# Kernel optimization log

Measured on AMD Instinct MI355X. Metric: run time of the kernel, lower is better.

Reference implementation:

```python
import jax, jax.numpy as jnp
import numpy as np

D_MODEL = 1024
N_HEADS = 16
D_HEAD = D_MODEL // N_HEADS
WINDOW = 256
DILATION = 1
GLOBAL_IDX = (0,)
NEG_INF = float('-inf')


def longformer_mask(seq_len):
    # Vectorized version of the original O(S^2) Python-loop mask builder.
    i = jnp.arange(seq_len)[:, None]
    j = jnp.arange(seq_len)[None, :]
    d = jnp.abs(i - j)
    window_ok = (d <= WINDOW) & (d % DILATION == 0)  # includes diagonal (d==0)
    is_global = jnp.zeros((seq_len,), dtype=bool).at[jnp.array(GLOBAL_IDX)].set(True)
    global_ok = is_global[:, None] | is_global[None, :]
    return jnp.where(window_ok | global_ok, 0.0, NEG_INF).astype(jnp.float32)


def setup_inputs() -> dict:
    key = jax.random.key(0)
    ks = jax.random.split(key, 9)
    s = 1.0 / np.sqrt(D_MODEL)
    inp = {'x': jax.random.normal(ks[0], (2, 2048, D_MODEL), dtype=jnp.float32)}
    for n, kw, kb in (('q', ks[1], ks[2]), ('k', ks[3], ks[4]), ('v', ks[5], ks[6]), ('o', ks[7], ks[8])):
        inp['W' + n] = jax.random.uniform(kw, (D_MODEL, D_MODEL), jnp.float32, -s, s)
        inp['b' + n] = jax.random.uniform(kb, (D_MODEL,), jnp.float32, -s, s)
    return inp


def reference(x, Wq, bq, Wk, bk, Wv, bv, Wo, bo):
    B, S, _ = x.shape
    scale = D_HEAD ** -0.5

    def split_heads(t):  # [B,S,D] -> [B,H,S,d]
        return t.reshape(B, S, N_HEADS, D_HEAD).transpose(0, 2, 1, 3)

    Q = split_heads(x @ Wq + bq)
    K = split_heads(x @ Wk + bk)
    V = split_heads(x @ Wv + bv)

    scores = jnp.einsum('bhqd,bhkd->bhqk', Q, K) * scale
    scores = scores + longformer_mask(S)[None, None]
    attn = jax.nn.softmax(scores, axis=-1)  # dropout is identity in eval
    out = jnp.einsum('bhqk,bhkd->bhqd', attn, V)
    out = out.transpose(0, 2, 1, 3).reshape(B, S, D_MODEL)
    return out @ Wo + bo
```

## Files before the change

kernel.cpp:

```cpp
#include <hip/hip_runtime.h>
#include <hip/hip_bf16.h>

typedef __attribute__((ext_vector_type(8))) short short8;
typedef __attribute__((ext_vector_type(4))) float floatx4;
typedef __attribute__((ext_vector_type(8))) _Float16 half8;
typedef __attribute__((ext_vector_type(4))) _Float16 half4;

using bf16 = __hip_bfloat16;
using fp16 = _Float16;

#define S_LEN 2048
#define DM 1024
#define NH 16
#define DH 64
#define WIN 256

__device__ __forceinline__ unsigned short f2b(float f) {
  __hip_bfloat16 h = __float2bfloat16(f);
  return *reinterpret_cast<unsigned short*>(&h);
}
__device__ __forceinline__ unsigned short f2h(float f) {
  fp16 h = (fp16)f;
  return *reinterpret_cast<unsigned short*>(&h);
}
__device__ __forceinline__ void lds_load16(void* lds, const void* gptr) {
  __builtin_amdgcn_global_load_lds(
      (const __attribute__((address_space(1))) unsigned int*)gptr,
      (__attribute__((address_space(3))) unsigned int*)lds, 16, 0, 0);
}

__global__ __launch_bounds__(256) void k_prep(const float* __restrict__ x,
                                              const float* __restrict__ W0,
                                              const float* __restrict__ W1,
                                              const float* __restrict__ W2,
                                              const float* __restrict__ W3,
                                              bf16* __restrict__ wT,
                                              ushort4* __restrict__ xb) {
  const int tx = threadIdx.x, ty = threadIdx.y;
  if (blockIdx.z == 4) {
    const int tid = ty * 32 + tx;
    const int blk = blockIdx.y * 32 + blockIdx.x;
    const float4* in4 = (const float4*)x;
    #pragma unroll
    for (int k = 0; k < 4; ++k) {
      int i = k * 262144 + blk * 256 + tid;
      float4 v = in4[i];
      ushort4 o;
      o.x = f2b(v.x); o.y = f2b(v.y); o.z = f2b(v.z); o.w = f2b(v.w);
      xb[i] = o;
    }
    return;
  }
  __shared__ float t[32][33];
  const float* W = (blockIdx.z == 0) ? W0 : (blockIdx.z == 1) ? W1 : (blockIdx.z == 2) ? W2 : W3;
  bf16* O = wT + (size_t)blockIdx.z * 1024 * 1024;
  int x0 = blockIdx.x * 32, y0 = blockIdx.y * 32;
  #pragma unroll
  for (int i = 0; i < 32; i += 8) t[ty + i][tx] = W[(size_t)(y0 + ty + i) * 1024 + x0 + tx];
  __syncthreads();
  #pragma unroll
  for (int i = 0; i < 32; i += 8)
    O[(size_t)(x0 + ty + i) * 1024 + y0 + tx] = __float2bfloat16(t[tx][ty + i]);
}

__global__ __launch_bounds__(512) void k_qkv(const bf16* __restrict__ A,
                                             const bf16* __restrict__ Bt,
                                             const float* __restrict__ bias_q,
                                             const float* __restrict__ bias_k,
                                             const float* __restrict__ bias_v,
                                             fp16* __restrict__ Qh, fp16* __restrict__ Kh,
                                             fp16* __restrict__ Vt) {
  __shared__ __align__(16) char lds[131072];
  const int tid = threadIdx.x;
  const int wave = tid >> 6, lane = tid & 63;
  const int ln = lane & 15, quad = lane >> 4;
  const int wr = wave >> 2, wc = wave & 3;

  const int gi = blockIdx.x;
  const int wg = (gi & 7) * 24 + (gi >> 3);
  const int mt = wg / 12, nt = wg % 12;

  auto mkF = [](int p) {
    int q = p ^ (((p >> 9) & 1) << 5);
    int sub = q >> 10;
    int w = q & 1023;
    return (((sub >> 1) << 4) + (w >> 6)) * 2048 + (sub & 1) * 64 + (w & 63);
  };
  const int F0 = mkF(tid * 16);
  const int F1 = mkF(8192 + tid * 16);
  const char* Ab = (const char*)A + (size_t)mt * 524288;
  const char* Bb = (const char*)Bt + (size_t)nt * 524288;

  auto stg = [&](int region, const char* g) {
    lds_load16(lds + region + wave * 1024, g + F0);
    lds_load16(lds + region + 8192 + wave * 1024, g + F1);
  };

  stg(0, Ab);
  stg(16384, Ab + 262144);
  stg(32768, Bb);
  stg(49152, Bb + 262144);
  stg(65536, Ab + 128);
  stg(65536 + 16384, Ab + 262144 + 128);
  stg(65536 + 32768, Bb + 128);
  stg(65536 + 49152, Bb + 262144 + 128);

  floatx4 acc[8][4];
  #pragma unroll
  for (int i = 0; i < 8; ++i)
    #pragma unroll
    for (int j = 0; j < 4; ++j) acc[i][j] = (floatx4){0.f, 0.f, 0.f, 0.f};

  const int lnq = ln * 64 + ((quad * 16) ^ ((ln & 8) << 2));
  const int aoff = wr * 16384 + lnq;
  const int boff = 32768 + (wc >> 1) * 16384 + (wc & 1) * 8192 + lnq;

  asm volatile("s_waitcnt vmcnt(8)" ::: "memory");
  __builtin_amdgcn_s_barrier();

  for (int t = 0; t < 16; ++t) {
    const char* bb = lds + ((t & 1) << 16);
    const int sreg = (t & 1) << 16;
    const char* gA = Ab + (t + 2) * 128;
    const char* gB = Bb + (t + 2) * 128;
    const bool pf = (t + 2 < 16);

    short8 a0[4][2], b0[4][2];
    #pragma unroll
    for (int m2 = 0; m2 < 4; ++m2)
      #pragma unroll
      for (int kk = 0; kk < 2; ++kk)
        a0[m2][kk] = *(const short8*)(bb + aoff + m2 * 2048 + kk * 1024);
    #pragma unroll
    for (int n2 = 0; n2 < 2; ++n2)
      #pragma unroll
      for (int kk = 0; kk < 2; ++kk)
        b0[n2][kk] = *(const short8*)(bb + boff + n2 * 2048 + kk * 1024);
    __builtin_amdgcn_s_barrier();
    __builtin_amdgcn_s_setprio(1);
    #pragma unroll
    for (int m2 = 0; m2 < 4; ++m2)
      #pragma unroll
      for (int n2 = 0; n2 < 2; ++n2) {
        acc[m2][n2] = __builtin_amdgcn_mfma_f32_16x16x32_bf16(a0[m2][0], b0[n2][0], acc[m2][n2], 0, 0, 0);
        acc[m2][n2] = __builtin_amdgcn_mfma_f32_16x16x32_bf16(a0[m2][1], b0[n2][1], acc[m2][n2], 0, 0, 0);
      }
    __builtin_amdgcn_s_setprio(0);
    __builtin_amdgcn_s_barrier();

    #pragma unroll
    for (int n2 = 2; n2 < 4; ++n2)
      #pragma unroll
      for (int kk = 0; kk < 2; ++kk)
        b0[n2][kk] = *(const short8*)(bb + boff + n2 * 2048 + kk * 1024);
    __builtin_amdgcn_s_barrier();
    __builtin_amdgcn_s_setprio(1);
    #pragma unroll
    for (int m2 = 0; m2 < 4; ++m2)
      #pragma unroll
      for (int n2 = 2; n2 < 4; ++n2) {
        acc[m2][n2] = __builtin_amdgcn_mfma_f32_16x16x32_bf16(a0[m2][0], b0[n2][0], acc[m2][n2], 0, 0, 0);
        acc[m2][n2] = __builtin_amdgcn_mfma_f32_16x16x32_bf16(a0[m2][1], b0[n2][1], acc[m2][n2], 0, 0, 0);
      }
    __builtin_amdgcn_s_setprio(0);
    __builtin_amdgcn_s_barrier();

    short8 a1[4][2];
    #pragma unroll
    for (int m2 = 0; m2 < 4; ++m2)
      #pragma unroll
      for (int kk = 0; kk < 2; ++kk)
        a1[m2][kk] = *(const short8*)(bb + aoff + (4 + m2) * 2048 + kk * 1024);
    if (pf) {
      stg(sreg + 32768, gB);
      stg(sreg + 49152, gB + 262144);
    }
    __builtin_amdgcn_s_barrier();
    __builtin_amdgcn_s_setprio(1);
    #pragma unroll
    for (int m2 = 0; m2 < 4; ++m2)
      #pragma unroll
      for (int n2 = 0; n2 < 2; ++n2) {
        acc[4 + m2][n2] = __builtin_amdgcn_mfma_f32_16x16x32_bf16(a1[m2][0], b0[n2][0], acc[4 + m2][n2], 0, 0, 0);
        acc[4 + m2][n2] = __builtin_amdgcn_mfma_f32_16x16x32_bf16(a1[m2][1], b0[n2][1], acc[4 + m2][n2], 0, 0, 0);
      }
    __builtin_amdgcn_s_setprio(0);
    __builtin_amdgcn_s_barrier();

    if (pf) {
      stg(sreg, gA);
      stg(sreg + 16384, gA + 262144);
      asm volatile("s_waitcnt vmcnt(8)" ::: "memory");
    } else {
      asm volatile("s_waitcnt vmcnt(0)" ::: "memory");
    }
    __builtin_amdgcn_s_barrier();
    __builtin_amdgcn_s_setprio(1);
    #pragma unroll
    for (int m2 = 0; m2 < 4; ++m2)
      #pragma unroll
      for (int n2 = 2; n2 < 4; ++n2) {
        acc[4 + m2][n2] = __builtin_amdgcn_mfma_f32_16x16x32_bf16(a1[m2][0], b0[n2][0], acc[4 + m2][n2], 0, 0, 0);
        acc[4 + m2][n2] = __builtin_amdgcn_mfma_f32_16x16x32_bf16(a1[m2][1], b0[n2][1], acc[4 + m2][n2], 0, 0, 0);
      }
    __builtin_amdgcn_s_setprio(0);
    __builtin_amdgcn_s_barrier();
  }

  const int g = nt >> 2;
  if (g == 2) {
    #pragma unroll
    for (int ni = 0; ni < 4; ++ni) {
      int nn = (nt & 3) * 256 + wc * 64 + ni * 16 + ln;
      int h = nn >> 6, dd = nn & 63;
      float bias = bias_v[nn];
      #pragma unroll
      for (int mi = 0; mi < 8; ++mi) {
        int m = mt * 256 + wr * 128 + mi * 16 + quad * 4;
        int b = m >> 11, s = m & 2047;
        ushort4 pk;
        pk.x = f2h(acc[mi][ni][0] + bias);
        pk.y = f2h(acc[mi][ni][1] + bias);
        pk.z = f2h(acc[mi][ni][2] + bias);
        pk.w = f2h(acc[mi][ni][3] + bias);
        *(ushort4*)&Vt[((size_t)((b * NH + h) * DH + dd)) * S_LEN + s] = pk;
      }
    }
  } else {
    const float* bp = (g == 0) ? bias_q : bias_k;
    fp16* og = (g == 0) ? Qh : Kh;
    #pragma unroll
    for (int ni = 0; ni < 4; ++ni) {
      int nn = (nt & 3) * 256 + wc * 64 + ni * 16 + ln;
      int h = nn >> 6, dd = nn & 63;
      float bias = bp[nn];
      #pragma unroll
      for (int mi = 0; mi < 8; ++mi) {
        #pragma unroll
        for (int r = 0; r < 4; ++r) {
          int m = mt * 256 + wr * 128 + mi * 16 + quad * 4 + r;
          int b = m >> 11, s = m & 2047;
          og[(size_t)((b * NH + h) * S_LEN + s) * DH + dd] = (fp16)(acc[mi][ni][r] + bias);
        }
      }
    }
  }
}

template <int MODE>
__global__ __launch_bounds__(256) void k_gemm(const bf16* __restrict__ A,
                                              const bf16* __restrict__ Bt,
                                              const float* __restrict__ bias_q,
                                              const float* __restrict__ bias_k,
                                              const float* __restrict__ bias_v,
                                              fp16* __restrict__ Qh, fp16* __restrict__ Kh,
                                              fp16* __restrict__ Vt, float* __restrict__ outF) {
  __shared__ __align__(16) bf16 As[2][128 * 32];
  __shared__ __align__(16) bf16 Bs[2][128 * 32];
  const int tid = threadIdx.x;
  const int wave = tid >> 6, lane = tid & 63;
  const int gi = blockIdx.x;
  const int xcd = gi & 7, grr = gi >> 3;
  const int m0 = (xcd * 4 + (grr & 3)) * 128;
  const int n0 = (grr >> 2) * 128;
  const int r0 = tid >> 2;
  const int cb = (tid & 3) * 16;
  const char* Ag = (const char*)A + (size_t)(m0 + r0) * 2048 + cb;
  const char* Bg = (const char*)Bt + (size_t)(n0 + r0) * 2048 + cb;
  char* As0W = (char*)&As[0][0] + wave * 1024;
  char* As1W = (char*)&As[1][0] + wave * 1024;
  char* Bs0W = (char*)&Bs[0][0] + wave * 1024;
  char* Bs1W = (char*)&Bs[1][0] + wave * 1024;
  const int wm = (wave & 1) * 64, wn = (wave >> 1) * 64;
  const int ln = lane & 15, quad = lane >> 4;

  floatx4 acc[4][4];
  #pragma unroll
  for (int i = 0; i < 4; i++)
    #pragma unroll
    for (int j = 0; j < 4; j++) acc[i][j] = (floatx4){0.f, 0.f, 0.f, 0.f};

  for (int k0 = 0; k0 < 1024; k0 += 64) {
    __syncthreads();
    lds_load16(As0W,        Ag + k0 * 2);
    lds_load16(As0W + 4096, Ag + 64 * 2048 + k0 * 2);
    lds_load16(As1W,        Ag + k0 * 2 + 64);
    lds_load16(As1W + 4096, Ag + 64 * 2048 + k0 * 2 + 64);
    lds_load16(Bs0W,        Bg + k0 * 2);
    lds_load16(Bs0W + 4096, Bg + 64 * 2048 + k0 * 2);
    lds_load16(Bs1W,        Bg + k0 * 2 + 64);
    lds_load16(Bs1W + 4096, Bg + 64 * 2048 + k0 * 2 + 64);
    __syncthreads();
    short8 af0[4], af1[4], bf0[4], bf1[4];
    #pragma unroll
    for (int mi = 0; mi < 4; mi++) {
      af0[mi] = *(const short8*)&As[0][(wm + mi * 16 + ln) * 32 + quad * 8];
      af1[mi] = *(const short8*)&As[1][(wm + mi * 16 + ln) * 32 + quad * 8];
    }
    #pragma unroll
    for (int ni = 0; ni < 4; ni++) {
      bf0[ni] = *(const short8*)&Bs[0][(wn + ni * 16 + ln) * 32 + quad * 8];
      bf1[ni] = *(const short8*)&Bs[1][(wn + ni * 16 + ln) * 32 + quad * 8];
    }
    #pragma unroll
    for (int mi = 0; mi < 4; mi++)
      #pragma unroll
      for (int ni = 0; ni < 4; ni++) {
        acc[mi][ni] = __builtin_amdgcn_mfma_f32_16x16x32_bf16(af0[mi], bf0[ni], acc[mi][ni], 0, 0, 0);
        acc[mi][ni] = __builtin_amdgcn_mfma_f32_16x16x32_bf16(af1[mi], bf1[ni], acc[mi][ni], 0, 0, 0);
      }
  }

  if constexpr (MODE == 0) {
    #pragma unroll
    for (int ni = 0; ni < 4; ni++) {
      int n = n0 + wn + ni * 16 + ln;
      int g = n >> 10, nn = n & 1023;
      int h = nn >> 6, dd = nn & 63;
      if (g == 2) {
        float bias = bias_v[nn];
        #pragma unroll
        for (int mi = 0; mi < 4; mi++) {
          int m = m0 + wm + mi * 16 + quad * 4;
          int b = m >> 11, s = m & 2047;
          ushort4 pk;
          pk.x = f2h(acc[mi][ni][0] + bias);
          pk.y = f2h(acc[mi][ni][1] + bias);
          pk.z = f2h(acc[mi][ni][2] + bias);
          pk.w = f2h(acc[mi][ni][3] + bias);
          *(ushort4*)&Vt[((size_t)(b * NH + h) * DH + dd) * S_LEN + s] = pk;
        }
      } else {
        const float* bp = (g == 0) ? bias_q : bias_k;
        fp16* og = (g == 0) ? Qh : Kh;
        float bias = bp[nn];
        #pragma unroll
        for (int mi = 0; mi < 4; mi++) {
          #pragma unroll
          for (int r = 0; r < 4; r++) {
            int m = m0 + wm + mi * 16 + quad * 4 + r;
            int b = m >> 11, s = m & 2047;
            og[(size_t)((b * NH + h) * S_LEN + s) * DH + dd] = (fp16)(acc[mi][ni][r] + bias);
          }
        }
      }
    }
  } else {
    #pragma unroll
    for (int ni = 0; ni < 4; ni++) {
      int n = n0 + wn + ni * 16 + ln;
      float bias = bias_q[n];
      #pragma unroll
      for (int mi = 0; mi < 4; mi++)
        #pragma unroll
        for (int r = 0; r < 4; r++) {
          int m = m0 + wm + mi * 16 + quad * 4 + r;
          outF[(size_t)m * 1024 + n] = acc[mi][ni][r] + bias;
        }
    }
  }
}

__global__ __launch_bounds__(256, 4) void k_attn(const fp16* __restrict__ Qh,
                                                 const fp16* __restrict__ Kh,
                                                 const fp16* __restrict__ Vt,
                                                 bf16* __restrict__ aout) {
  __shared__ __align__(16) fp16 KsL[2][64 * 72];
  __shared__ __align__(16) fp16 VsL[2][64 * 72];

  const int i = blockIdx.x;
  const int xcd = i & 7, rr = i >> 3;
  const int bh = xcd * 4 + (rr & 3);
  const int tile = rr >> 2;
  const int b = bh >> 4, h = bh & 15;
  const size_t base = (size_t)bh * S_LEN * DH;
  const fp16* Qp = Qh + base;
  const fp16* Kp = Kh + base;
  const fp16* Vp = Vt + base;
  const float SC2 = 0.18033688011112042f;
  const int tid = threadIdx.x;

  if (tile == 32) {
    float* sP = (float*)&KsL[0][0];
    float* oR = (float*)&VsL[0][0];
    float* red = (float*)&VsL[1][0];
    const int wv = tid >> 6, lane = tid & 63;
    const int g = lane >> 3, e8 = lane & 7;
    const half8 q0t = *(const half8*)(Qp + e8 * 8);
    float lsum = 0.f;
    for (int it = 0; it < 64; ++it) {
      int grp = wv * 64 + it;
      const half8 kv = *(const half8*)(Kp + (size_t)(grp * 8 + g) * DH + e8 * 8);
      float p = 0.f;
      #pragma unroll
      for (int e = 0; e < 8; ++e) p += (float)q0t[e] * (float)kv[e];
      p += __shfl_xor(p, 1, 64);
      p += __shfl_xor(p, 2, 64);
      p += __shfl_xor(p, 4, 64);
      p = exp2f(fmaf(p, SC2, -8.f));
      if (e8 == 0) sP[grp * 8 + g] = p;
      lsum += p;
    }
    #pragma unroll
    for (int off = 1; off < 64; off <<= 1) lsum += __shfl_xor(lsum, off, 64);
    if (lane == 0) red[wv] = lsum;
    __syncthreads();
    const float ltot = (red[0] + red[1] + red[2] + red[3]) * 0.125f;
    const int d = tid & 63, qu = tid >> 6;
    float o = 0.f;
    for (int j0 = qu * 512; j0 < qu * 512 + 512; j0 += 8) {
      half8 vv = *(const half8*)(Vp + (size_t)d * S_LEN + j0);
      #pragma unroll
      for (int e = 0; e < 8; ++e) o += sP[j0 + e] * (float)vv[e];
    }
    oR[tid] = o;
    __syncthreads();
    if (tid < 64) {
      float oo = oR[tid] + oR[tid + 64] + oR[tid + 128] + oR[tid + 192];
      aout[(size_t)(b * S_LEN) * DM + h * DH + tid] = __float2bfloat16(oo / ltot);
    }
    return;
  }

  const int w = tid >> 6, lane = tid & 63;
  const int ln = lane & 15, quad = lane >> 4;
  const int qb = tile * 64;
  const int qw = qb + w * 16;

  const half8 bq0 = *(const half8*)(Qp + (size_t)(qw + ln) * DH + quad * 8);
  const half8 bq1 = *(const half8*)(Qp + (size_t)(qw + ln) * DH + 32 + quad * 8);

  floatx4 acc[4];
  float l_i;

  {
    const half8 k0a = *(const half8*)(Kp + quad * 8);
    const half8 k0b = *(const half8*)(Kp + 32 + quad * 8);
    float s0 = 0.f;
    #pragma unroll
    for (int e = 0; e < 8; ++e)
      s0 += (float)bq0[e] * (float)k0a[e] + (float)bq1[e] * (float)k0b[e];
    s0 += __shfl_xor(s0, 16, 64);
    s0 += __shfl_xor(s0, 32, 64);
    float p0 = exp2f(fmaf(s0, SC2, -8.f));
    l_i = (quad == 0) ? p0 : 0.f;
    #pragma unroll
    for (int dt = 0; dt < 4; ++dt)
      #pragma unroll
      for (int r = 0; r < 4; ++r)
        acc[dt][r] = p0 * (float)Vp[(size_t)(dt * 16 + quad * 4 + r) * S_LEN];
  }

  int cs = qb - WIN; if (cs < 0) cs = 0;
  int ce = qb + 64 + WIN; if (ce > S_LEN) ce = S_LEN;

  const int f0 = tid, f1 = tid + 256;
  const int r0s = f0 >> 3, c0s = (f0 & 7) * 8;
  const int r1s = f1 >> 3, c1s = (f1 & 7) * 8;

  uint4 kreg0, kreg1, vreg0, vreg1;
  auto stage_load = [&](int c) {
    kreg0 = *(const uint4*)(Kp + (size_t)(c + r0s) * DH + c0s);
    kreg1 = *(const uint4*)(Kp + (size_t)(c + r1s) * DH + c1s);
    vreg0 = *(const uint4*)(Vp + (size_t)r0s * S_LEN + c + c0s);
    vreg1 = *(const uint4*)(Vp + (size_t)r1s * S_LEN + c + c1s);
  };
  auto stage_write = [&](int buf) {
    *(uint4*)&KsL[buf][r0s * 72 + c0s] = kreg0;
    *(uint4*)&KsL[buf][r1s * 72 + c1s] = kreg1;
    *(uint4*)&VsL[buf][r0s * 72 + c0s] = vreg0;
    *(uint4*)&VsL[buf][r1s * 72 + c1s] = vreg1;
  };

  auto compute = [&](int c, int buf) {
    floatx4 s[4];
    #pragma unroll
    for (int jt = 0; jt < 4; ++jt) {
      half8 k0 = *(const half8*)&KsL[buf][(jt * 16 + ln) * 72 + quad * 8];
      half8 k1 = *(const half8*)&KsL[buf][(jt * 16 + ln) * 72 + 32 + quad * 8];
      floatx4 z = (floatx4){0.f, 0.f, 0.f, 0.f};
      z = __builtin_amdgcn_mfma_f32_16x16x32_f16(k0, bq0, z, 0, 0, 0);
      s[jt] = __builtin_amdgcn_mfma_f32_16x16x32_f16(k1, bq1, z, 0, 0, 0);
    }
    half4 v01[8];
    #pragma unroll
    for (int dt = 0; dt < 2; ++dt)
      #pragma unroll
      for (int jt = 0; jt < 4; ++jt)
        v01[dt * 4 + jt] =
            *(const half4*)&VsL[buf][(dt * 16 + ln) * 72 + jt * 16 + quad * 4];
    const bool full_in = (c != 0) && (c >= qw - 241) && (c <= qw + 193);
    half4 Pt[4];
    if (full_in) {
      #pragma unroll
      for (int jt = 0; jt < 4; ++jt)
        #pragma unroll
        for (int r = 0; r < 4; ++r) {
          float pe = exp2f(fmaf(s[jt][r], SC2, -8.f));
          Pt[jt][r] = (fp16)pe;
          l_i += pe;
        }
    } else {
      const int q = qw + ln;
      #pragma unroll
      for (int jt = 0; jt < 4; ++jt) {
        #pragma unroll
        for (int r = 0; r < 4; ++r) {
          int j = c + jt * 16 + quad * 4 + r;
          int dq = q - j;
          bool ok = (dq <= WIN && dq >= -WIN) && (j != 0);
          float pe = ok ? exp2f(fmaf(s[jt][r], SC2, -8.f)) : 0.f;
          Pt[jt][r] = (fp16)pe;
          l_i += pe;
        }
      }
    }
    half4 v23[8];
    #pragma unroll
    for (int dt = 0; dt < 2; ++dt)
      #pragma unroll
      for (int jt = 0; jt < 4; ++jt)
        v23[dt * 4 + jt] =
            *(const half4*)&VsL[buf][((dt + 2) * 16 + ln) * 72 + jt * 16 + quad * 4];
    #pragma unroll
    for (int jt = 0; jt < 4; ++jt) {
      acc[0] = __builtin_amdgcn_mfma_f32_16x16x16f16(v01[jt], Pt[jt], acc[0], 0, 0, 0);
      acc[1] = __builtin_amdgcn_mfma_f32_16x16x16f16(v01[4 + jt], Pt[jt], acc[1], 0, 0, 0);
    }
    #pragma unroll
    for (int jt = 0; jt < 4; ++jt) {
      acc[2] = __builtin_amdgcn_mfma_f32_16x16x16f16(v23[jt], Pt[jt], acc[2], 0, 0, 0);
      acc[3] = __builtin_amdgcn_mfma_f32_16x16x16f16(v23[4 + jt], Pt[jt], acc[3], 0, 0, 0);
    }
  };

  stage_load(cs);
  stage_write(0);
  __syncthreads();
  int buf = 0;
  for (int c = cs; c < ce; c += 64) {
    const bool hasnext = (c + 64 < ce);
    if (hasnext) stage_load(c + 64);
    compute(c, buf);
    if (hasnext) stage_write(buf ^ 1);
    __syncthreads();
    buf ^= 1;
  }

  float lt = l_i;
  lt += __shfl_xor(lt, 16, 64);
  lt += __shfl_xor(lt, 32, 64);
  const float inv = 1.0f / lt;
  const int q = qw + ln;
  if (q != 0) {
    #pragma unroll
    for (int dt = 0; dt < 4; ++dt) {
      ushort4 pk;
      pk.x = f2b(acc[dt][0] * inv);
      pk.y = f2b(acc[dt][1] * inv);
      pk.z = f2b(acc[dt][2] * inv);
      pk.w = f2b(acc[dt][3] * inv);
      *(ushort4*)&aout[(size_t)(b * S_LEN + q) * DM + h * DH + dt * 16 + quad * 4] = pk;
    }
  }
}

extern "C" void kernel_launch(void* const* d_in, const int* in_sizes, int n_in,
                              void* d_out, int out_size, void* d_ws, size_t ws_size,
                              hipStream_t stream) {
  const float* x  = (const float*)d_in[0];
  const float* Wq = (const float*)d_in[1];
  const float* bq = (const float*)d_in[2];
  const float* Wk = (const float*)d_in[3];
  const float* bk = (const float*)d_in[4];
  const float* Wv = (const float*)d_in[5];
  const float* bv = (const float*)d_in[6];
  const float* Wo = (const float*)d_in[7];
  const float* bo = (const float*)d_in[8];
  float* out = (float*)d_out;

  const size_t SEG = (size_t)4096 * 1024;
  bf16* xb = (bf16*)d_ws;
  bf16* wT = xb + SEG;
  fp16* Qh = (fp16*)(wT + SEG);
  fp16* Kh = Qh + SEG;
  fp16* Vt = Kh + SEG;
  bf16* ao = (bf16*)(Vt + SEG);

  k_prep<<<dim3(32, 32, 5), dim3(32, 8), 0, stream>>>(x, Wq, Wk, Wv, Wo, wT, (ushort4*)xb);
  k_qkv<<<dim3(192), dim3(512), 0, stream>>>(xb, wT, bq, bk, bv, Qh, Kh, Vt);
  k_attn<<<dim3(1056), dim3(256), 0, stream>>>(Qh, Kh, Vt, ao);
  k_gemm<1><<<dim3(256), dim3(256), 0, stream>>>(ao, wT + (size_t)3 * 1024 * 1024, bo,
                                                 nullptr, nullptr, nullptr, nullptr, nullptr, out);
}
```

Measured before the change: 190.3 us.

## Double attention query tile to 128 with 512 threads and fold global row into tile 0

The attention kernel now runs 512-thread blocks that each cover 128 queries instead of 64, so every K/V chunk staged in LDS is reused by eight waves rather than four, and the grid shrinks from 1056 to 512 blocks. The separate block that computed the global query row is removed; that work now runs at the end of tile 0's blocks, using eight waves. Probability packing switches to cvt_pkrtz. Tile-0 blocks carry extra tail work, which may create load imbalance, and the total block count drops.

```diff
diff --git a/kernel.cpp b/kernel.cpp
--- a/kernel.cpp
+++ b/kernel.cpp
@@ -5,6 +5,7 @@
 typedef __attribute__((ext_vector_type(4))) float floatx4;
 typedef __attribute__((ext_vector_type(8))) _Float16 half8;
 typedef __attribute__((ext_vector_type(4))) _Float16 half4;
+typedef __attribute__((ext_vector_type(2))) __fp16 fp16x2_raw;
 
 using bf16 = __hip_bfloat16;
 using fp16 = _Float16;
@@ -22,6 +23,12 @@
 __device__ __forceinline__ unsigned short f2h(float f) {
   fp16 h = (fp16)f;
   return *reinterpret_cast<unsigned short*>(&h);
+}
+__device__ __forceinline__ half4 pack4(float a, float b, float c, float d) {
+  union { half4 h4; fp16x2_raw h2[2]; } u;
+  u.h2[0] = __builtin_amdgcn_cvt_pkrtz(a, b);
+  u.h2[1] = __builtin_amdgcn_cvt_pkrtz(c, d);
+  return u.h4;
 }
 __device__ __forceinline__ void lds_load16(void* lds, const void* gptr) {
   __builtin_amdgcn_global_load_lds(
@@ -361,7 +368,7 @@
   }
 }
 
-__global__ __launch_bounds__(256, 4) void k_attn(const fp16* __restrict__ Qh,
+__global__ __launch_bounds__(512, 4) void k_attn(const fp16* __restrict__ Qh,
                                                  const fp16* __restrict__ Kh,
                                                  const fp16* __restrict__ Vt,
                                                  bf16* __restrict__ aout) {
@@ -380,51 +387,9 @@
   const float SC2 = 0.18033688011112042f;
   const int tid = threadIdx.x;
 
-  if (tile == 32) {
-    float* sP = (float*)&KsL[0][0];
-    float* oR = (float*)&VsL[0][0];
-    float* red = (float*)&VsL[1][0];
-    const int wv = tid >> 6, lane = tid & 63;
-    const int g = lane >> 3, e8 = lane & 7;
-    const half8 q0t = *(const half8*)(Qp + e8 * 8);
-    float lsum = 0.f;
-    for (int it = 0; it < 64; ++it) {
-      int grp = wv * 64 + it;
-      const half8 kv = *(const half8*)(Kp + (size_t)(grp * 8 + g) * DH + e8 * 8);
-      float p = 0.f;
-      #pragma unroll
-      for (int e = 0; e < 8; ++e) p += (float)q0t[e] * (float)kv[e];
-      p += __shfl_xor(p, 1, 64);
-      p += __shfl_xor(p, 2, 64);
-      p += __shfl_xor(p, 4, 64);
-      p = exp2f(fmaf(p, SC2, -8.f));
-      if (e8 == 0) sP[grp * 8 + g] = p;
-      lsum += p;
-    }
-    #pragma unroll
-    for (int off = 1; off < 64; off <<= 1) lsum += __shfl_xor(lsum, off, 64);
-    if (lane == 0) red[wv] = lsum;
-    __syncthreads();
-    const float ltot = (red[0] + red[1] + red[2] + red[3]) * 0.125f;
-    const int d = tid & 63, qu = tid >> 6;
-    float o = 0.f;
-    for (int j0 = qu * 512; j0 < qu * 512 + 512; j0 += 8) {
-      half8 vv = *(const half8*)(Vp + (size_t)d * S_LEN + j0);
-      #pragma unroll
-      for (int e = 0; e < 8; ++e) o += sP[j0 + e] * (float)vv[e];
-    }
-    oR[tid] = o;
-    __syncthreads();
-    if (tid < 64) {
-      float oo = oR[tid] + oR[tid + 64] + oR[tid + 128] + oR[tid + 192];
-      aout[(size_t)(b * S_LEN) * DM + h * DH + tid] = __float2bfloat16(oo / ltot);
-    }
-    return;
-  }
-
   const int w = tid >> 6, lane = tid & 63;
   const int ln = lane & 15, quad = lane >> 4;
-  const int qb = tile * 64;
+  const int qb = tile * 128;
   const int qw = qb + w * 16;
 
   const half8 bq0 = *(const half8*)(Qp + (size_t)(qw + ln) * DH + quad * 8);
@@ -452,24 +417,18 @@
   }
 
   int cs = qb - WIN; if (cs < 0) cs = 0;
-  int ce = qb + 64 + WIN; if (ce > S_LEN) ce = S_LEN;
-
-  const int f0 = tid, f1 = tid + 256;
-  const int r0s = f0 >> 3, c0s = (f0 & 7) * 8;
-  const int r1s = f1 >> 3, c1s = (f1 & 7) * 8;
-
-  uint4 kreg0, kreg1, vreg0, vreg1;
+  int ce = qb + 128 + WIN; if (ce > S_LEN) ce = S_LEN;
+
+  const int rs = tid >> 3, cls = (tid & 7) * 8;
+
+  uint4 kreg, vreg;
   auto stage_load = [&](int c) {
-    kreg0 = *(const uint4*)(Kp + (size_t)(c + r0s) * DH + c0s);
-    kreg1 = *(const uint4*)(Kp + (size_t)(c + r1s) * DH + c1s);
-    vreg0 = *(const uint4*)(Vp + (size_t)r0s * S_LEN + c + c0s);
-    vreg1 = *(const uint4*)(Vp + (size_t)r1s * S_LEN + c + c1s);
+    kreg = *(const uint4*)(Kp + (size_t)(c + rs) * DH + cls);
+    vreg = *(const uint4*)(Vp + (size_t)rs * S_LEN + c + cls);
   };
   auto stage_write = [&](int buf) {
-    *(uint4*)&KsL[buf][r0s * 72 + c0s] = kreg0;
-    *(uint4*)&KsL[buf][r1s * 72 + c1s] = kreg1;
-    *(uint4*)&VsL[buf][r0s * 72 + c0s] = vreg0;
-    *(uint4*)&VsL[buf][r1s * 72 + c1s] = vreg1;
+    *(uint4*)&KsL[buf][rs * 72 + cls] = kreg;
+    *(uint4*)&VsL[buf][rs * 72 + cls] = vreg;
   };
 
   auto compute = [&](int c, int buf) {
@@ -493,26 +452,28 @@
     half4 Pt[4];
     if (full_in) {
       #pragma unroll
-      for (int jt = 0; jt < 4; ++jt)
-        #pragma unroll
-        for (int r = 0; r < 4; ++r) {
-          float pe = exp2f(fmaf(s[jt][r], SC2, -8.f));
-          Pt[jt][r] = (fp16)pe;
-          l_i += pe;
-        }
+      for (int jt = 0; jt < 4; ++jt) {
+        float p0 = exp2f(fmaf(s[jt][0], SC2, -8.f));
+        float p1 = exp2f(fmaf(s[jt][1], SC2, -8.f));
+        float p2 = exp2f(fmaf(s[jt][2], SC2, -8.f));
+        float p3 = exp2f(fmaf(s[jt][3], SC2, -8.f));
+        Pt[jt] = pack4(p0, p1, p2, p3);
+        l_i += (p0 + p1) + (p2 + p3);
+      }
     } else {
       const int q = qw + ln;
       #pragma unroll
       for (int jt = 0; jt < 4; ++jt) {
+        float pv[4];
         #pragma unroll
         for (int r = 0; r < 4; ++r) {
           int j = c + jt * 16 + quad * 4 + r;
           int dq = q - j;
           bool ok = (dq <= WIN && dq >= -WIN) && (j != 0);
-          float pe = ok ? exp2f(fmaf(s[jt][r], SC2, -8.f)) : 0.f;
-          Pt[jt][r] = (fp16)pe;
-          l_i += pe;
+          pv[r] = ok ? exp2f(fmaf(s[jt][r], SC2, -8.f)) : 0.f;
         }
+        Pt[jt] = pack4(pv[0], pv[1], pv[2], pv[3]);
+        l_i += (pv[0] + pv[1]) + (pv[2] + pv[3]);
       }
     }
     half4 v23[8];
@@ -547,20 +508,64 @@
     buf ^= 1;
   }
 
-  float lt = l_i;
-  lt += __shfl_xor(lt, 16, 64);
-  lt += __shfl_xor(lt, 32, 64);
-  const float inv = 1.0f / lt;
-  const int q = qw + ln;
-  if (q != 0) {
-    #pragma unroll
-    for (int dt = 0; dt < 4; ++dt) {
-      ushort4 pk;
-      pk.x = f2b(acc[dt][0] * inv);
-      pk.y = f2b(acc[dt][1] * inv);
-      pk.z = f2b(acc[dt][2] * inv);
-      pk.w = f2b(acc[dt][3] * inv);
-      *(ushort4*)&aout[(size_t)(b * S_LEN + q) * DM + h * DH + dt * 16 + quad * 4] = pk;
+  {
+    float lt = l_i;
+    lt += __shfl_xor(lt, 16, 64);
+    lt += __shfl_xor(lt, 32, 64);
+    const float inv = 1.0f / lt;
+    const int q = qw + ln;
+    if (q != 0) {
+      #pragma unroll
+      for (int dt = 0; dt < 4; ++dt) {
+        ushort4 pk;
+        pk.x = f2b(acc[dt][0] * inv);
+        pk.y = f2b(acc[dt][1] * inv);
+        pk.z = f2b(acc[dt][2] * inv);
+        pk.w = f2b(acc[dt][3] * inv);
+        *(ushort4*)&aout[(size_t)(b * S_LEN + q) * DM + h * DH + dt * 16 + quad * 4] = pk;
+      }
+    }
+  }
+
+  if (tile == 0) {
+    float* sP = (float*)&KsL[0][0];
+    float* oR = (float*)&VsL[0][0];
+    float* red = (float*)&VsL[1][0];
+    const int g2 = lane >> 3, e8 = lane & 7;
+    const half8 q0t = *(const half8*)(Qp + e8 * 8);
+    float lsum = 0.f;
+    for (int it = 0; it < 32; ++it) {
+      int grp = w * 32 + it;
+      const half8 kv = *(const half8*)(Kp + (size_t)(grp * 8 + g2) * DH + e8 * 8);
+      float p = 0.f;
+      #pragma unroll
+      for (int e = 0; e < 8; ++e) p += (float)q0t[e] * (float)kv[e];
+      p += __shfl_xor(p, 1, 64);
+      p += __shfl_xor(p, 2, 64);
+      p += __shfl_xor(p, 4, 64);
+      p = exp2f(fmaf(p, SC2, -8.f));
+      if (e8 == 0) sP[grp * 8 + g2] = p;
+      lsum += p;
+    }
+    #pragma unroll
+    for (int off = 1; off < 64; off <<= 1) lsum += __shfl_xor(lsum, off, 64);
+    if (lane == 0) red[w] = lsum;
+    __syncthreads();
+    const float ltot = (red[0] + red[1] + red[2] + red[3] +
+                        red[4] + red[5] + red[6] + red[7]) * 0.125f;
+    const int d = tid & 63, qu = tid >> 6;
+    float o = 0.f;
+    for (int j0 = qu * 256; j0 < qu * 256 + 256; j0 += 8) {
+      half8 vv = *(const half8*)(Vp + (size_t)d * S_LEN + j0);
+      #pragma unroll
+      for (int e = 0; e < 8; ++e) o += sP[j0 + e] * (float)vv[e];
+    }
+    oR[tid] = o;
+    __syncthreads();
+    if (tid < 64) {
+      float oo = oR[tid] + oR[tid + 64] + oR[tid + 128] + oR[tid + 192] +
+                 oR[tid + 256] + oR[tid + 320] + oR[tid + 384] + oR[tid + 448];
+      aout[(size_t)(b * S_LEN) * DM + h * DH + tid] = __float2bfloat16(oo / ltot);
     }
   }
 }
@@ -589,7 +594,7 @@
 
   k_prep<<<dim3(32, 32, 5), dim3(32, 8), 0, stream>>>(x, Wq, Wk, Wv, Wo, wT, (ushort4*)xb);
   k_qkv<<<dim3(192), dim3(512), 0, stream>>>(xb, wT, bq, bk, bv, Qh, Kh, Vt);
-  k_attn<<<dim3(1056), dim3(256), 0, stream>>>(Qh, Kh, Vt, ao);
+  k_attn<<<dim3(512), dim3(512), 0, stream>>>(Qh, Kh, Vt, ao);
   k_gemm<1><<<dim3(256), dim3(256), 0, stream>>>(ao, wT + (size_t)3 * 1024 * 1024, bo,
                                                  nullptr, nullptr, nullptr, nullptr, nullptr, out);
 }
```

Measured after the change: 185.8 us. 1.02x faster.
